# Kernel optimization log

Measured on AMD Instinct MI355X. Metric: run time of the kernel, lower is better.

The kernel has to match this reference:

```python
import jax, jax.numpy as jnp
import numpy as np

N_ENTITY = 100000
N_RELATION = 64
DIM = 16
N_HOP = 2
N_MEM = 32
N_NODES = 16384


def setup_inputs() -> dict:
    key = jax.random.key(0)
    ks = jax.random.split(key, 7)
    return {
        "nodes": jax.random.randint(ks[0], (N_NODES,), 0, N_ENTITY),
        "memories_h": jax.random.randint(ks[1], (N_HOP, N_NODES, N_MEM), 0, N_ENTITY),
        "memories_r": jax.random.randint(ks[2], (N_HOP, N_NODES, N_MEM), 0, N_RELATION),
        "memories_t": jax.random.randint(ks[3], (N_HOP, N_NODES, N_MEM), 0, N_ENTITY),
        "entity_emb": jax.random.normal(ks[4], (N_ENTITY, DIM), jnp.float32) * 0.1,
        "relation_emb": jax.random.normal(ks[5], (N_RELATION, DIM * DIM), jnp.float32) * 0.1,
        "W": jax.random.normal(ks[6], (DIM, DIM), jnp.float32) * 0.1,
    }


def reference(nodes, memories_h, memories_r, memories_t, entity_emb, relation_emb, W):
    # item embeddings for the query nodes: [N, D]
    item = entity_emb[nodes]
    o_list = []
    for hop in range(N_HOP):  # small fixed hop count (2)
        h = entity_emb[memories_h[hop]]                                  # [N, M, D]
        r = relation_emb[memories_r[hop]].reshape(-1, N_MEM, DIM, DIM)   # [N, M, D, D]
        t = entity_emb[memories_t[hop]]                                  # [N, M, D]
        # Rh = R @ h : [N, M, D]
        Rh = jnp.einsum('nmde,nme->nmd', r, h)
        # attention over the n_memory slots (softmax dim=0 per node in original)
        probs = jax.nn.softmax(jnp.einsum('nmd,nd->nm', Rh, item), axis=1)
        # weighted sum of tails: [N, D]
        o = jnp.einsum('nm,nmd->nd', probs, t)
        # item_update_mode == 'plus_transform': Linear(dim, dim, bias=False)
        item = (item + o) @ W.T
        o_list.append(o)
    # Faithful to the original torch in-place semantics: at hop 0 the line
    # `kg_feature += o_list[0]` doubles o0 in place; the final result for
    # n_hop=2 is therefore o1 + 2*o0.
    return o_list[1] + 2.0 * o_list[0]
```

## Files before the change

### kernel.cpp

```cpp
#include <hip/hip_runtime.h>

#define NE     100000
#define NR     64
#define DIM    16
#define NHOP   2
#define NMEM   32
#define NNODES 16384

#define WPITCH 20

typedef __attribute__((ext_vector_type(2))) _Float16 half2_t;

static __device__ __forceinline__ half2_t as_h2(unsigned u) {
    union { unsigned i; half2_t h; } c; c.i = u; return c.h;
}

static __device__ __forceinline__ float qdot2(unsigned u, unsigned ip, float q) {
#if __has_builtin(__builtin_amdgcn_fdot2)
    return __builtin_amdgcn_fdot2(as_h2(u), as_h2(ip), q, false);
#else
    half2_t a = as_h2(u), b = as_h2(ip);
    return q + (float)a.x * (float)b.x + (float)a.y * (float)b.y;
#endif
}

static __device__ __forceinline__ float dpp_sum16(float v) {
    union { int i; float f; } a, b;
    a.f = v;
    b.i = __builtin_amdgcn_update_dpp(0, a.i, 0xB1,  0xf, 0xf, true); a.f += b.f;
    b.i = __builtin_amdgcn_update_dpp(0, a.i, 0x4E,  0xf, 0xf, true); a.f += b.f;
    b.i = __builtin_amdgcn_update_dpp(0, a.i, 0x124, 0xf, 0xf, true); a.f += b.f;
    b.i = __builtin_amdgcn_update_dpp(0, a.i, 0x128, 0xf, 0xf, true); a.f += b.f;
    return a.f;
}

static __device__ __forceinline__ float bcast(float v, int l) {
    return __int_as_float(__builtin_amdgcn_readlane(__float_as_int(v), l));
}

static __device__ __forceinline__ unsigned short f2h(float f) {
    union { _Float16 h; unsigned short s; } c; c.h = (_Float16)f; return c.s;
}
static __device__ __forceinline__ unsigned pack2h(float a, float b) {
    union { _Float16 h[2]; unsigned u; } c;
    c.h[0] = (_Float16)a; c.h[1] = (_Float16)b;
    return c.u;
}

extern "C" __global__ void __launch_bounds__(256)
ent_quant_kernel(const float* __restrict__ ent, _Float16* __restrict__ et, int n4) {
    int i = blockIdx.x * 256 + threadIdx.x;
    if (i < n4) {
        float4 v = ((const float4*)ent)[i];
        union { _Float16 h[4]; unsigned long long u; } c;
        c.h[0] = (_Float16)v.x; c.h[1] = (_Float16)v.y;
        c.h[2] = (_Float16)v.z; c.h[3] = (_Float16)v.w;
        *(unsigned long long*)(et + 4 * (long long)i) = c.u;
    }
}

extern "C" __global__ void __launch_bounds__(512, 8)
ripple_kernel(const int* __restrict__ nodes,
              const int* __restrict__ mh,
              const int* __restrict__ mr,
              const int* __restrict__ mt,
              const _Float16* __restrict__ et,
              const float* __restrict__ rel,
              const float* __restrict__ W,
              float* __restrict__ out)
{
    __shared__ __align__(16) unsigned short rt[NR * 256];
    __shared__ __align__(16) float ws[DIM * WPITCH];

    const int tid = threadIdx.x;

    {
        const float4* rel4 = (const float4*)rel;
        #pragma unroll
        for (int i = 0; i < 8; ++i) {
            int vidx = i * 512 + tid;
            float4 v = rel4[vidx];
            int k0 = vidx * 4;
            int r  = k0 >> 8;
            int k  = k0 & 255;
            int d  = k >> 4;
            int e0 = k & 15;
            int phys = ((d >> 2) + (e0 >> 2)) & 3;
            unsigned short* p = &rt[r * 256 + e0 * 16 + phys * 4 + (d & 3)];
            p[0]  = f2h(v.x);
            p[16] = f2h(v.y);
            p[32] = f2h(v.z);
            p[48] = f2h(v.w);
        }
        if (tid < 256) ws[(tid >> 4) * WPITCH + (tid & 15)] = W[tid];
    }
    __syncthreads();

    const int lane = tid & 63;
    const int wid  = tid >> 6;
    const int g    = lane >> 4;
    const int e    = lane & 15;
    const int n    = blockIdx.x * 8 + wid;

    int voff[4];
    {
        const int s = e >> 2;
        #pragma unroll
        for (int j = 0; j < 4; ++j)
            voff[j] = e * 32 + (((j + s) & 3) << 3);
    }

    float item    = (float)et[nodes[n] * DIM + e];
    float out_acc = 0.f;

    #pragma unroll
    for (int hop = 0; hop < NHOP; ++hop) {
        unsigned ip[8];
        #pragma unroll
        for (int j = 0; j < 8; ++j)
            ip[j] = pack2h(bcast(item, 2 * j), bcast(item, 2 * j + 1));

        const int ibase = hop * (NNODES * NMEM) + n * NMEM + g * 8;
        int hi[8], ri[8], ti[8];
        {
            const int4* p;
            p = (const int4*)(mh + ibase); *(int4*)&hi[0] = p[0]; *(int4*)&hi[4] = p[1];
            p = (const int4*)(mr + ibase); *(int4*)&ri[0] = p[0]; *(int4*)&ri[4] = p[1];
            p = (const int4*)(mt + ibase); *(int4*)&ti[0] = p[0]; *(int4*)&ti[4] = p[1];
        }

        float hv[8];
        #pragma unroll
        for (int it = 0; it < 8; ++it) hv[it] = (float)et[hi[it] * DIM + e];

        float Z = 0.f, o = 0.f;
        #pragma unroll
        for (int it = 0; it < 8; ++it) {
            float tv = (float)et[ti[it] * DIM + e];
            const char* rbase = (const char*)rt + (ri[it] << 9);
            float q = 0.f;
            #pragma unroll
            for (int j = 0; j < 4; ++j) {
                uint2 u = *(const uint2*)(rbase + voff[j]);
                q = qdot2(u.x, ip[2 * j + 0], q);
                q = qdot2(u.y, ip[2 * j + 1], q);
            }
            float sc = dpp_sum16(q * hv[it]);
            float ex = __expf(sc);
            Z += ex;
            o += ex * tv;
        }
        Z += __shfl_xor(Z, 16);
        Z += __shfl_xor(Z, 32);
        o += __shfl_xor(o, 16);
        o += __shfl_xor(o, 32);
        o *= 1.f / Z;

        out_acc += (hop == 0) ? 2.f * o : o;

        const float v = item + o;
        float nit = 0.f;
        const float4* wr = (const float4*)&ws[e * WPITCH];
        #pragma unroll
        for (int j = 0; j < 4; ++j) {
            float4 w = wr[j];
            nit += w.x * bcast(v, 4 * j + 0) + w.y * bcast(v, 4 * j + 1)
                 + w.z * bcast(v, 4 * j + 2) + w.w * bcast(v, 4 * j + 3);
        }
        item = nit;
    }

    if (lane < 16) out[n * DIM + e] = out_acc;
}

extern "C" void kernel_launch(void* const* d_in, const int* in_sizes, int n_in,
                              void* d_out, int out_size, void* d_ws, size_t ws_size,
                              hipStream_t stream) {
    const int*   nodes = (const int*)d_in[0];
    const int*   mh    = (const int*)d_in[1];
    const int*   mr    = (const int*)d_in[2];
    const int*   mt    = (const int*)d_in[3];
    const float* ent   = (const float*)d_in[4];
    const float* rel   = (const float*)d_in[5];
    const float* W     = (const float*)d_in[6];
    float*       out   = (float*)d_out;
    _Float16*    et    = (_Float16*)d_ws;

    const int n4 = NE * DIM / 4;
    ent_quant_kernel<<<(n4 + 255) / 256, 256, 0, stream>>>(ent, et, n4);

    dim3 grid(NNODES / 8);
    dim3 block(512);
    ripple_kernel<<<grid, block, 0, stream>>>(nodes, mh, mr, mt, et, rel, W, out);
}
```

Before: 100.2 us.

## Pre-swizzle relation table once, prefetch all gathers before LDS fill

A prep kernel now converts the relation matrices to fp16 in the swizzled layout once, in global memory, alongside the entity quantization. The main kernel copies that table straight into LDS with float4 loads, and it issues all memory-index and entity gathers for both hops before the LDS store and barrier, so their latency overlaps the table fill. Blocks shrink to 4 waves (256 threads) with more blocks, which doubles how often each block has to fill the 32KB LDS table and raises register pressure from the preloaded arrays.

New measurement: 100.0 us. No clear change (-0.2%).

```diff
diff --git a/kernel.cpp b/kernel.cpp
--- a/kernel.cpp
+++ b/kernel.cpp
@@ -8,13 +8,14 @@
 #define NNODES 16384
 
 #define WPITCH 20
+#define ET_BYTES (NE * DIM * 2)
+#define NB_ET  ((NE * DIM / 4 + 255) / 256)
 
 typedef __attribute__((ext_vector_type(2))) _Float16 half2_t;
 
 static __device__ __forceinline__ half2_t as_h2(unsigned u) {
     union { unsigned i; half2_t h; } c; c.i = u; return c.h;
 }
-
 static __device__ __forceinline__ float qdot2(unsigned u, unsigned ip, float q) {
 #if __has_builtin(__builtin_amdgcn_fdot2)
     return __builtin_amdgcn_fdot2(as_h2(u), as_h2(ip), q, false);
@@ -23,7 +24,6 @@
     return q + (float)a.x * (float)b.x + (float)a.y * (float)b.y;
 #endif
 }
-
 static __device__ __forceinline__ float dpp_sum16(float v) {
     union { int i; float f; } a, b;
     a.f = v;
@@ -33,11 +33,9 @@
     b.i = __builtin_amdgcn_update_dpp(0, a.i, 0x128, 0xf, 0xf, true); a.f += b.f;
     return a.f;
 }
-
 static __device__ __forceinline__ float bcast(float v, int l) {
     return __int_as_float(__builtin_amdgcn_readlane(__float_as_int(v), l));
 }
-
 static __device__ __forceinline__ unsigned short f2h(float f) {
     union { _Float16 h; unsigned short s; } c; c.h = (_Float16)f; return c.s;
 }
@@ -48,59 +46,100 @@
 }
 
 extern "C" __global__ void __launch_bounds__(256)
-ent_quant_kernel(const float* __restrict__ ent, _Float16* __restrict__ et, int n4) {
-    int i = blockIdx.x * 256 + threadIdx.x;
-    if (i < n4) {
-        float4 v = ((const float4*)ent)[i];
-        union { _Float16 h[4]; unsigned long long u; } c;
-        c.h[0] = (_Float16)v.x; c.h[1] = (_Float16)v.y;
-        c.h[2] = (_Float16)v.z; c.h[3] = (_Float16)v.w;
-        *(unsigned long long*)(et + 4 * (long long)i) = c.u;
-    }
-}
-
-extern "C" __global__ void __launch_bounds__(512, 8)
+prep_kernel(const float* __restrict__ ent, const float* __restrict__ rel,
+            _Float16* __restrict__ et, unsigned short* __restrict__ rtg, int n4)
+{
+    const int b = blockIdx.x, tid = threadIdx.x;
+    if (b < NB_ET) {
+        int i = b * 256 + tid;
+        if (i < n4) {
+            float4 v = ((const float4*)ent)[i];
+            union { _Float16 h[4]; unsigned long long u; } c;
+            c.h[0] = (_Float16)v.x; c.h[1] = (_Float16)v.y;
+            c.h[2] = (_Float16)v.z; c.h[3] = (_Float16)v.w;
+            *(unsigned long long*)(et + 4 * (long long)i) = c.u;
+        }
+    } else {
+        int j = (b - NB_ET) * 256 + tid;
+        const float4* rel4 = (const float4*)rel;
+        #pragma unroll
+        for (int k = 0; k < 4; ++k) {
+            int vidx = k * 1024 + j;
+            float4 v = rel4[vidx];
+            int k0 = vidx * 4;
+            int r  = k0 >> 8;
+            int kk = k0 & 255;
+            int d  = kk >> 4;
+            int e0 = kk & 15;
+            int phys = ((d >> 2) + (e0 >> 2)) & 3;
+            unsigned short* p = &rtg[r * 256 + e0 * 16 + phys * 4 + (d & 3)];
+            p[0]  = f2h(v.x);
+            p[16] = f2h(v.y);
+            p[32] = f2h(v.z);
+            p[48] = f2h(v.w);
+        }
+    }
+}
+
+extern "C" __global__ void __launch_bounds__(256, 4)
 ripple_kernel(const int* __restrict__ nodes,
               const int* __restrict__ mh,
               const int* __restrict__ mr,
               const int* __restrict__ mt,
               const _Float16* __restrict__ et,
-              const float* __restrict__ rel,
+              const unsigned short* __restrict__ rtg,
               const float* __restrict__ W,
               float* __restrict__ out)
 {
     __shared__ __align__(16) unsigned short rt[NR * 256];
     __shared__ __align__(16) float ws[DIM * WPITCH];
 
-    const int tid = threadIdx.x;
-
-    {
-        const float4* rel4 = (const float4*)rel;
-        #pragma unroll
-        for (int i = 0; i < 8; ++i) {
-            int vidx = i * 512 + tid;
-            float4 v = rel4[vidx];
-            int k0 = vidx * 4;
-            int r  = k0 >> 8;
-            int k  = k0 & 255;
-            int d  = k >> 4;
-            int e0 = k & 15;
-            int phys = ((d >> 2) + (e0 >> 2)) & 3;
-            unsigned short* p = &rt[r * 256 + e0 * 16 + phys * 4 + (d & 3)];
-            p[0]  = f2h(v.x);
-            p[16] = f2h(v.y);
-            p[32] = f2h(v.z);
-            p[48] = f2h(v.w);
-        }
-        if (tid < 256) ws[(tid >> 4) * WPITCH + (tid & 15)] = W[tid];
-    }
-    __syncthreads();
-
+    const int tid  = threadIdx.x;
     const int lane = tid & 63;
     const int wid  = tid >> 6;
     const int g    = lane >> 4;
     const int e    = lane & 15;
-    const int n    = blockIdx.x * 8 + wid;
+    const int n    = blockIdx.x * 4 + wid;
+
+    const int ib0 = 0 * (NNODES * NMEM) + n * NMEM + g * 8;
+    const int ib1 = 1 * (NNODES * NMEM) + n * NMEM + g * 8;
+    int hi0[8], ri0[8], ti0[8], hi1[8], ri1[8], ti1[8];
+    {
+        const int4* p;
+        p = (const int4*)(mh + ib0); *(int4*)&hi0[0] = p[0]; *(int4*)&hi0[4] = p[1];
+        p = (const int4*)(mr + ib0); *(int4*)&ri0[0] = p[0]; *(int4*)&ri0[4] = p[1];
+        p = (const int4*)(mt + ib0); *(int4*)&ti0[0] = p[0]; *(int4*)&ti0[4] = p[1];
+        p = (const int4*)(mh + ib1); *(int4*)&hi1[0] = p[0]; *(int4*)&hi1[4] = p[1];
+        p = (const int4*)(mr + ib1); *(int4*)&ri1[0] = p[0]; *(int4*)&ri1[4] = p[1];
+        p = (const int4*)(mt + ib1); *(int4*)&ti1[0] = p[0]; *(int4*)&ti1[4] = p[1];
+    }
+    const int nd = nodes[n];
+
+    float4 stg[8];
+    {
+        const float4* src = (const float4*)rtg;
+        #pragma unroll
+        for (int i = 0; i < 8; ++i) stg[i] = src[i * 256 + tid];
+    }
+    const float wv = W[tid];
+
+    float item = (float)et[nd * DIM + e];
+    float hv0[8], tv0[8], hv1[8], tv1[8];
+    #pragma unroll
+    for (int it = 0; it < 8; ++it) {
+        hv0[it] = (float)et[hi0[it] * DIM + e];
+        tv0[it] = (float)et[ti0[it] * DIM + e];
+        hv1[it] = (float)et[hi1[it] * DIM + e];
+        tv1[it] = (float)et[ti1[it] * DIM + e];
+    }
+
+    {
+        float4* dst = (float4*)rt;
+        #pragma unroll
+        for (int i = 0; i < 8; ++i) dst[i * 256 + tid] = stg[i];
+        ws[(tid >> 4) * WPITCH + (tid & 15)] = wv;
+    }
+    __syncthreads();
 
     int voff[4];
     {
@@ -110,33 +149,22 @@
             voff[j] = e * 32 + (((j + s) & 3) << 3);
     }
 
-    float item    = (float)et[nodes[n] * DIM + e];
     float out_acc = 0.f;
 
     #pragma unroll
     for (int hop = 0; hop < NHOP; ++hop) {
+        const int*   ri = hop ? ri1 : ri0;
+        const float* hv = hop ? hv1 : hv0;
+        const float* tv = hop ? tv1 : tv0;
+
         unsigned ip[8];
         #pragma unroll
         for (int j = 0; j < 8; ++j)
             ip[j] = pack2h(bcast(item, 2 * j), bcast(item, 2 * j + 1));
 
-        const int ibase = hop * (NNODES * NMEM) + n * NMEM + g * 8;
-        int hi[8], ri[8], ti[8];
-        {
-            const int4* p;
-            p = (const int4*)(mh + ibase); *(int4*)&hi[0] = p[0]; *(int4*)&hi[4] = p[1];
-            p = (const int4*)(mr + ibase); *(int4*)&ri[0] = p[0]; *(int4*)&ri[4] = p[1];
-            p = (const int4*)(mt + ibase); *(int4*)&ti[0] = p[0]; *(int4*)&ti[4] = p[1];
-        }
-
-        float hv[8];
-        #pragma unroll
-        for (int it = 0; it < 8; ++it) hv[it] = (float)et[hi[it] * DIM + e];
-
         float Z = 0.f, o = 0.f;
         #pragma unroll
         for (int it = 0; it < 8; ++it) {
-            float tv = (float)et[ti[it] * DIM + e];
             const char* rbase = (const char*)rt + (ri[it] << 9);
             float q = 0.f;
             #pragma unroll
@@ -148,7 +176,7 @@
             float sc = dpp_sum16(q * hv[it]);
             float ex = __expf(sc);
             Z += ex;
-            o += ex * tv;
+            o += ex * tv[it];
         }
         Z += __shfl_xor(Z, 16);
         Z += __shfl_xor(Z, 32);
@@ -184,12 +212,14 @@
     const float* rel   = (const float*)d_in[5];
     const float* W     = (const float*)d_in[6];
     float*       out   = (float*)d_out;
-    _Float16*    et    = (_Float16*)d_ws;
+
+    _Float16*       et  = (_Float16*)d_ws;
+    unsigned short* rtg = (unsigned short*)((char*)d_ws + ET_BYTES);
 
     const int n4 = NE * DIM / 4;
-    ent_quant_kernel<<<(n4 + 255) / 256, 256, 0, stream>>>(ent, et, n4);
-
-    dim3 grid(NNODES / 8);
-    dim3 block(512);
-    ripple_kernel<<<grid, block, 0, stream>>>(nodes, mh, mr, mt, et, rel, W, out);
-}
+    prep_kernel<<<NB_ET + 4, 256, 0, stream>>>(ent, rel, et, rtg, n4);
+
+    dim3 grid(NNODES / 4);
+    dim3 block(256);
+    ripple_kernel<<<grid, block, 0, stream>>>(nodes, mh, mr, mt, et, rtg, W, out);
+}
```
